# Kernel tuning notes

Hardware: AMD Instinct MI355X
Metric: run time of the kernel (lower is better)

Reference implementation:

```python
import jax, jax.numpy as jnp
import numpy as np

D_MODEL = 128
N_HEADS = 8
HEAD_DIM = D_MODEL // N_HEADS
N_NODES = 50000
N_EDGES = 640000


def setup_inputs() -> dict:
    key = jax.random.key(0)
    ks = jax.random.split(key, 10)
    sd = 1.0 / np.sqrt(D_MODEL)
    return {
        "node_embeds": jax.random.normal(ks[0], (N_NODES, D_MODEL), dtype=jnp.float32),
        "edge_index": jax.random.randint(ks[1], (2, N_EDGES), 0, N_NODES, dtype=jnp.int64),
        "Wq": jax.random.uniform(ks[2], (D_MODEL, D_MODEL), jnp.float32, -sd, sd),
        "bq": jax.random.uniform(ks[3], (D_MODEL,), jnp.float32, -sd, sd),
        "Wk": jax.random.uniform(ks[4], (D_MODEL, D_MODEL), jnp.float32, -sd, sd),
        "bk": jax.random.uniform(ks[5], (D_MODEL,), jnp.float32, -sd, sd),
        "Wv": jax.random.uniform(ks[6], (D_MODEL, D_MODEL), jnp.float32, -sd, sd),
        "bv": jax.random.uniform(ks[7], (D_MODEL,), jnp.float32, -sd, sd),
        "gamma": jnp.ones((D_MODEL,), jnp.float32),
        "beta": jnp.zeros((D_MODEL,), jnp.float32),
    }


def reference(node_embeds, edge_index, Wq, bq, Wk, bk, Wv, bv, gamma, beta):
    num_nodes = node_embeds.shape[0]
    rows, cols = edge_index[0], edge_index[1]
    src = node_embeds[rows]  # (E, d)
    tgt = node_embeds[cols]  # (E, d)
    q = (src @ Wq.T + bq).reshape(-1, N_HEADS, HEAD_DIM)
    k = (tgt @ Wk.T + bk).reshape(-1, N_HEADS, HEAD_DIM)
    v = (tgt @ Wv.T + bv).reshape(-1, N_HEADS, HEAD_DIM)
    att = jnp.einsum('ehd,ehd->eh', q, k) / jnp.sqrt(jnp.float32(HEAD_DIM))
    exp_att = jnp.exp(jnp.clip(att, -10.0, 10.0))  # (E, h)
    att_sum = jax.ops.segment_sum(exp_att, rows, num_segments=num_nodes)  # (N, h)
    att_norm = exp_att / (att_sum[rows] + 1e-8)
    weighted_v = (att_norm[..., None] * v).reshape(-1, D_MODEL)  # (E, d)
    out = jax.ops.segment_sum(weighted_v, rows, num_segments=num_nodes)
    out = out + node_embeds
    # LayerNorm, eps=1e-6
    mu = jnp.mean(out, axis=-1, keepdims=True)
    var = jnp.mean(jnp.square(out - mu), axis=-1, keepdims=True)
    out = (out - mu) * jax.lax.rsqrt(var + 1e-6) * gamma + beta
    return out
```

## Files before the change

kernel.cpp:

```cpp
#include <hip/hip_runtime.h>
#include <hip/hip_bf16.h>
#include <cstdint>

#define D_MODEL 128
#define N_HEADS 8
#define HEAD_DIM 16

typedef __attribute__((ext_vector_type(8))) short bf16x8;
typedef __attribute__((ext_vector_type(4))) float f32x4;

static __device__ __forceinline__ float b2f(unsigned short u) {
  unsigned int x = ((unsigned int)u) << 16;
  return __builtin_bit_cast(float, x);
}
static __device__ __forceinline__ unsigned short f2b(float f) {
  __hip_bfloat16 h = __float2bfloat16(f);
  return __builtin_bit_cast(unsigned short, h);
}

__global__ __launch_bounds__(256) void cvtw_kernel(
    const float* __restrict__ Wq, const float* __restrict__ Wk,
    const float* __restrict__ Wv, unsigned short* __restrict__ Wb)
{
  const int wb = blockIdx.x;
  const int m  = wb >> 3;
  const float* src = (m == 0) ? Wq : (m == 1) ? Wk : Wv;
  unsigned short* dst = Wb + (size_t)m * 16384;
  const int base = ((wb & 7) * 256 + threadIdx.x) * 8;
  const float4 a = reinterpret_cast<const float4*>(src + base)[0];
  const float4 c = reinterpret_cast<const float4*>(src + base)[1];
  unsigned short tmp[8];
  tmp[0] = f2b(a.x); tmp[1] = f2b(a.y); tmp[2] = f2b(a.z); tmp[3] = f2b(a.w);
  tmp[4] = f2b(c.x); tmp[5] = f2b(c.y); tmp[6] = f2b(c.z); tmp[7] = f2b(c.w);
  reinterpret_cast<uint4*>(dst + base)[0] = *reinterpret_cast<uint4*>(tmp);
}

__global__ __launch_bounds__(128) void qkv_mfma(
    const float* __restrict__ X, const unsigned short* __restrict__ Wb,
    const float* __restrict__ bq, const float* __restrict__ bk,
    const float* __restrict__ bv,
    unsigned short* __restrict__ Qo, unsigned short* __restrict__ Ko,
    unsigned short* __restrict__ Vo, int N)
{
  __shared__ unsigned short Wl[128 * 128];
  const int t    = threadIdx.x;
  const int wave = t >> 6;
  const int l    = t & 63;
  const int lr   = l & 15;
  const int lg   = l >> 4;
  const int nw   = blockIdx.x * 64 + wave * 32;

  bf16x8 a[2][4];
  #pragma unroll
  for (int ng = 0; ng < 2; ++ng) {
    const int arow = nw + ng * 16 + lr;
    if (arow < N) {
      const float* xp = X + (size_t)arow * D_MODEL + lg * 8;
      #pragma unroll
      for (int ks = 0; ks < 4; ++ks) {
        const float4 f0 = reinterpret_cast<const float4*>(xp + ks * 32)[0];
        const float4 f1 = reinterpret_cast<const float4*>(xp + ks * 32)[1];
        unsigned short tm[8];
        tm[0] = f2b(f0.x); tm[1] = f2b(f0.y); tm[2] = f2b(f0.z); tm[3] = f2b(f0.w);
        tm[4] = f2b(f1.x); tm[5] = f2b(f1.y); tm[6] = f2b(f1.z); tm[7] = f2b(f1.w);
        a[ng][ks] = *reinterpret_cast<bf16x8*>(tm);
      }
    } else {
      #pragma unroll
      for (int ks = 0; ks < 4; ++ks) a[ng][ks] = bf16x8{0,0,0,0,0,0,0,0};
    }
  }

  const float* biases[3] = {bq, bk, bv};
  unsigned short* outs[3] = {Qo, Ko, Vo};

  #pragma unroll 1
  for (int m = 0; m < 3; ++m) {
    __syncthreads();
    {
      const uint4* wsrc = reinterpret_cast<const uint4*>(Wb + (size_t)m * 16384);
      uint4* wl4 = reinterpret_cast<uint4*>(Wl);
      #pragma unroll
      for (int i = 0; i < 16; ++i) {
        const int cg = i * 128 + t;
        const int r  = cg >> 4;
        const int j  = cg & 15;
        wl4[r * 16 + (j ^ (r & 7))] = wsrc[cg];
      }
    }
    __syncthreads();

    unsigned short* __restrict__ O = outs[m];
    const float* __restrict__ bias = biases[m];
    float bias8[8];
    #pragma unroll
    for (int c = 0; c < 8; ++c) bias8[c] = bias[c * 16 + lr];

    #pragma unroll
    for (int c = 0; c < 8; ++c) {
      const int row = c * 16 + lr;
      bf16x8 w[4];
      #pragma unroll
      for (int ks = 0; ks < 4; ++ks) {
        const int j = ks * 4 + lg;
        w[ks] = *reinterpret_cast<const bf16x8*>(
            Wl + ((row * 16 + (j ^ (row & 7))) * 8));
      }
      #pragma unroll
      for (int ng = 0; ng < 2; ++ng) {
        f32x4 acc = {bias8[c], bias8[c], bias8[c], bias8[c]};
        #pragma unroll
        for (int ks = 0; ks < 4; ++ks)
          acc = __builtin_amdgcn_mfma_f32_16x16x32_bf16(a[ng][ks], w[ks], acc, 0, 0, 0);
        #pragma unroll
        for (int r = 0; r < 4; ++r) {
          const int orow = nw + ng * 16 + lg * 4 + r;
          if (orow < N) O[(size_t)orow * D_MODEL + c * 16 + lr] = f2b(acc[r]);
        }
      }
    }
  }
}

__global__ __launch_bounds__(256) void hist_kernel(
    const int* __restrict__ rows, int* __restrict__ cnt, int E)
{
  const int e = blockIdx.x * 256 + threadIdx.x;
  if (e < E) atomicAdd(&cnt[rows[e]], 1);
}

__global__ __launch_bounds__(256) void partial_kernel(
    const int* __restrict__ cnt, int* __restrict__ bsum, int N)
{
  __shared__ int wsum[4];
  const int t = threadIdx.x;
  const int base = blockIdx.x * 1024 + t * 4;
  int s = 0;
  #pragma unroll
  for (int i = 0; i < 4; ++i)
    if (base + i < N) s += cnt[base + i];
  #pragma unroll
  for (int off = 32; off > 0; off >>= 1) s += __shfl_xor(s, off, 64);
  if ((t & 63) == 0) wsum[t >> 6] = s;
  __syncthreads();
  if (t == 0) bsum[blockIdx.x] = wsum[0] + wsum[1] + wsum[2] + wsum[3];
}

__global__ __launch_bounds__(256) void scansums_kernel(
    const int* __restrict__ bsum, int* __restrict__ boff, int nb)
{
  __shared__ int p[256];
  __shared__ int carry_s;
  const int t = threadIdx.x;
  if (t == 0) carry_s = 0;
  __syncthreads();
  for (int c0 = 0; c0 < nb; c0 += 256) {
    const int v = (c0 + t < nb) ? bsum[c0 + t] : 0;
    p[t] = v;
    __syncthreads();
    for (int off = 1; off < 256; off <<= 1) {
      const int other = (t >= off) ? p[t - off] : 0;
      __syncthreads();
      p[t] += other;
      __syncthreads();
    }
    const int carry = carry_s;
    if (c0 + t < nb) boff[c0 + t] = carry + p[t] - v;
    __syncthreads();
    if (t == 0) carry_s = carry + p[255];
    __syncthreads();
  }
}

__global__ __launch_bounds__(256) void emit_kernel(
    const int* __restrict__ cnt, const int* __restrict__ boff,
    int* __restrict__ row_ptr, int* __restrict__ row_cur, int N, int E)
{
  __shared__ int psum[256];
  const int t = threadIdx.x;
  const int base = blockIdx.x * 1024 + t * 4;
  int v[4];
  #pragma unroll
  for (int i = 0; i < 4; ++i)
    v[i] = (base + i < N) ? cnt[base + i] : 0;
  const int local = v[0] + v[1] + v[2] + v[3];
  psum[t] = local;
  __syncthreads();
  for (int off = 1; off < 256; off <<= 1) {
    const int other = (t >= off) ? psum[t - off] : 0;
    __syncthreads();
    psum[t] += other;
    __syncthreads();
  }
  int pre = boff[blockIdx.x] + psum[t] - local;
  #pragma unroll
  for (int i = 0; i < 4; ++i) {
    const int idx = base + i;
    if (idx < N) {
      row_ptr[idx] = pre;
      row_cur[idx] = pre;
      pre += v[i];
    }
  }
  if (blockIdx.x == 0 && t == 0) row_ptr[N] = E;
}

__global__ __launch_bounds__(256) void scatter_kernel(
    const int* __restrict__ rows, const int* __restrict__ cols,
    int* __restrict__ row_cur, int* __restrict__ csr_cols, int E)
{
  const int e = blockIdx.x * 256 + threadIdx.x;
  if (e >= E) return;
  const int pos = atomicAdd(&row_cur[rows[e]], 1);
  csr_cols[pos] = cols[e];
}

__global__ __launch_bounds__(256) void fused_kernel(
    const unsigned short* __restrict__ Q, const unsigned short* __restrict__ K,
    const unsigned short* __restrict__ V, const float* __restrict__ X,
    const int* __restrict__ row_ptr, const int* __restrict__ csr_cols,
    const float* __restrict__ gamma, const float* __restrict__ beta,
    float* __restrict__ out, int N)
{
  __shared__ float lds[4][576];
  const int wv = threadIdx.x >> 6;
  const int n  = blockIdx.x * 4 + wv;
  if (n >= N) return;
  const int l  = threadIdx.x & 63;
  const int h  = l & 7;
  const int g  = l >> 3;
  const int hd = l >> 3;

  unsigned* __restrict__ Vu = reinterpret_cast<unsigned*>(lds[wv]);
  float*    __restrict__ El = lds[wv] + 512;

  float qf[16];
  {
    const unsigned short* qp = Q + (size_t)n * D_MODEL + h * HEAD_DIM;
    const bf16x8 q0 = *reinterpret_cast<const bf16x8*>(qp);
    const bf16x8 q1 = *reinterpret_cast<const bf16x8*>(qp + 8);
    #pragma unroll
    for (int i = 0; i < 8; ++i) {
      qf[i]     = b2f((unsigned short)q0[i]);
      qf[8 + i] = b2f((unsigned short)q1[i]);
    }
  }

  float accx = 0.f, accy = 0.f, dlane = 0.f;
  const int e0 = row_ptr[n];
  const int e1 = row_ptr[n + 1];

  const int rcol = (l & 7) * 64;
  const int rrot = (l >> 3) + 4 * (l & 7);

  for (int eb = e0; eb < e1; eb += 8) {
    const int  eg    = eb + g;
    const bool valid = eg < e1;
    const int  c     = valid ? csr_cols[eg] : 0;

    const unsigned short* kp = K + (size_t)c * D_MODEL + h * HEAD_DIM;
    const unsigned short* vp = V + (size_t)c * D_MODEL + h * HEAD_DIM;
    const bf16x8 k0 = *reinterpret_cast<const bf16x8*>(kp);
    const bf16x8 k1 = *reinterpret_cast<const bf16x8*>(kp + 8);
    const bf16x8 v0 = *reinterpret_cast<const bf16x8*>(vp);
    const bf16x8 v1 = *reinterpret_cast<const bf16x8*>(vp + 8);

    float s = 0.f;
    #pragma unroll
    for (int i = 0; i < 8; ++i) {
      s = fmaf(qf[i],     b2f((unsigned short)k0[i]), s);
      s = fmaf(qf[8 + i], b2f((unsigned short)k1[i]), s);
    }
    s *= 0.25f;
    s = fminf(fmaxf(s, -10.f), 10.f);
    const float ea = valid ? __expf(s) : 0.f;
    dlane += ea;

    El[l] = ea;
    {
      const uint4 u0 = __builtin_bit_cast(uint4, v0);
      const uint4 u1 = __builtin_bit_cast(uint4, v1);
      Vu[0 * 64 + ((l +  0) & 63)] = u0.x;
      Vu[1 * 64 + ((l +  4) & 63)] = u0.y;
      Vu[2 * 64 + ((l +  8) & 63)] = u0.z;
      Vu[3 * 64 + ((l + 12) & 63)] = u0.w;
      Vu[4 * 64 + ((l + 16) & 63)] = u1.x;
      Vu[5 * 64 + ((l + 20) & 63)] = u1.y;
      Vu[6 * 64 + ((l + 24) & 63)] = u1.z;
      Vu[7 * 64 + ((l + 28) & 63)] = u1.w;
    }
    __builtin_amdgcn_sched_barrier(0);

    #pragma unroll
    for (int j = 0; j < 8; ++j) {
      const float    aj = El[j * 8 + hd];
      const unsigned vv = Vu[rcol + ((j * 8 + rrot) & 63)];
      accx = fmaf(aj, b2f((unsigned short)(vv & 0xffffu)), accx);
      accy = fmaf(aj, b2f((unsigned short)(vv >> 16)), accy);
    }
    __builtin_amdgcn_sched_barrier(0);
  }

  dlane += __shfl_xor(dlane, 8,  64);
  dlane += __shfl_xor(dlane, 16, 64);
  dlane += __shfl_xor(dlane, 32, 64);
  const float denom = __shfl(dlane, hd, 64);

  const float inv = 1.f / (denom + 1e-8f);
  const float2 x = reinterpret_cast<const float2*>(X + (size_t)n * D_MODEL)[l];
  const float a0 = accx * inv + x.x;
  const float a1 = accy * inv + x.y;

  float sm = a0 + a1;
  float ss = a0 * a0 + a1 * a1;
  #pragma unroll
  for (int off = 32; off > 0; off >>= 1) {
    sm += __shfl_xor(sm, off, 64);
    ss += __shfl_xor(ss, off, 64);
  }
  const float mean = sm * (1.f / 128.f);
  const float var  = ss * (1.f / 128.f) - mean * mean;
  const float rs   = rsqrtf(var + 1e-6f);
  const float2 gm = reinterpret_cast<const float2*>(gamma)[l];
  const float2 bt = reinterpret_cast<const float2*>(beta)[l];
  float2 o;
  o.x = (a0 - mean) * rs * gm.x + bt.x;
  o.y = (a1 - mean) * rs * gm.y + bt.y;
  reinterpret_cast<float2*>(out + (size_t)n * D_MODEL)[l] = o;
}

extern "C" void kernel_launch(void* const* d_in, const int* in_sizes, int n_in,
                              void* d_out, int out_size, void* d_ws, size_t ws_size,
                              hipStream_t stream)
{
  const float* X     = (const float*)d_in[0];
  const int*   ei    = (const int*)  d_in[1];
  const float* Wq    = (const float*)d_in[2];
  const float* bq    = (const float*)d_in[3];
  const float* Wk    = (const float*)d_in[4];
  const float* bk    = (const float*)d_in[5];
  const float* Wv    = (const float*)d_in[6];
  const float* bv    = (const float*)d_in[7];
  const float* gamma = (const float*)d_in[8];
  const float* beta  = (const float*)d_in[9];

  const int N = in_sizes[0] / D_MODEL;
  const int E = in_sizes[1] / 2;
  const int* rows = ei;
  const int* cols = ei + E;

  const size_t nd = (size_t)N * D_MODEL;
  unsigned short* Wb = (unsigned short*)d_ws;
  unsigned short* Qb = Wb + 3 * 16384;
  unsigned short* Kb = Qb + nd;
  unsigned short* Vb = Kb + nd;
  int* row_cnt  = (int*)(Vb + nd);
  int* row_ptr  = row_cnt + N;
  int* row_cur  = row_ptr + N + 1;
  int* csr_cols = row_cur + N;
  int* bsum     = csr_cols + E;
  int* boff     = bsum + ((N + 1023) / 1024) + 1;

  const int nb = (N + 1023) / 1024;

  hipMemsetAsync(row_cnt, 0, (size_t)N * sizeof(int), stream);

  cvtw_kernel<<<24, 256, 0, stream>>>(Wq, Wk, Wv, Wb);

  hist_kernel<<<(E + 255) / 256, 256, 0, stream>>>(rows, row_cnt, E);
  partial_kernel<<<nb, 256, 0, stream>>>(row_cnt, bsum, N);
  scansums_kernel<<<1, 256, 0, stream>>>(bsum, boff, nb);
  emit_kernel<<<nb, 256, 0, stream>>>(row_cnt, boff, row_ptr, row_cur, N, E);
  scatter_kernel<<<(E + 255) / 256, 256, 0, stream>>>(rows, cols, row_cur, csr_cols, E);

  qkv_mfma<<<(N + 63) / 64, 128, 0, stream>>>(
      X, Wb, bq, bk, bv, Qb, Kb, Vb, N);

  fused_kernel<<<(N + 3) / 4, 256, 0, stream>>>(
      Qb, Kb, Vb, X, row_ptr, csr_cols, gamma, beta, (float*)d_out, N);
}
```

Before: 164.0 us.

## Software-pipeline edge gathers with prefetch of next K/V and column indices

Restructures the per-node edge loop so the K/V gathers for the next batch of 8 edges, and the column indices two batches ahead, are issued before the current batch's LDS exchange and accumulation. The LDS scratch is doubled and ping-ponged between iterations. The aim is to hide the global-memory gather latency behind compute within a single wave. It costs more registers for the in-flight K/V vectors, which may reduce occupancy, and loads past the last batch fall back to row 0.

```diff
diff --git a/kernel.cpp b/kernel.cpp
--- a/kernel.cpp
+++ b/kernel.cpp
@@ -222,7 +222,7 @@
     const float* __restrict__ gamma, const float* __restrict__ beta,
     float* __restrict__ out, int N)
 {
-  __shared__ float lds[4][576];
+  __shared__ float lds[4][2][576];
   const int wv = threadIdx.x >> 6;
   const int n  = blockIdx.x * 4 + wv;
   if (n >= N) return;
@@ -231,8 +231,8 @@
   const int g  = l >> 3;
   const int hd = l >> 3;
 
-  unsigned* __restrict__ Vu = reinterpret_cast<unsigned*>(lds[wv]);
-  float*    __restrict__ El = lds[wv] + 512;
+  float* buf0 = lds[wv][0];
+  float* buf1 = lds[wv][1];
 
   float qf[16];
   {
@@ -253,52 +253,82 @@
   const int rcol = (l & 7) * 64;
   const int rrot = (l >> 3) + 4 * (l & 7);
 
-  for (int eb = e0; eb < e1; eb += 8) {
-    const int  eg    = eb + g;
-    const bool valid = eg < e1;
-    const int  c     = valid ? csr_cols[eg] : 0;
-
-    const unsigned short* kp = K + (size_t)c * D_MODEL + h * HEAD_DIM;
-    const unsigned short* vp = V + (size_t)c * D_MODEL + h * HEAD_DIM;
-    const bf16x8 k0 = *reinterpret_cast<const bf16x8*>(kp);
-    const bf16x8 k1 = *reinterpret_cast<const bf16x8*>(kp + 8);
-    const bf16x8 v0 = *reinterpret_cast<const bf16x8*>(vp);
-    const bf16x8 v1 = *reinterpret_cast<const bf16x8*>(vp + 8);
-
-    float s = 0.f;
-    #pragma unroll
-    for (int i = 0; i < 8; ++i) {
-      s = fmaf(qf[i],     b2f((unsigned short)k0[i]), s);
-      s = fmaf(qf[8 + i], b2f((unsigned short)k1[i]), s);
-    }
-    s *= 0.25f;
-    s = fminf(fmaxf(s, -10.f), 10.f);
-    const float ea = valid ? __expf(s) : 0.f;
-    dlane += ea;
-
-    El[l] = ea;
+  if (e0 < e1) {
+    int cA;
+    bf16x8 kA0, kA1, vA0, vA1;
     {
-      const uint4 u0 = __builtin_bit_cast(uint4, v0);
-      const uint4 u1 = __builtin_bit_cast(uint4, v1);
-      Vu[0 * 64 + ((l +  0) & 63)] = u0.x;
-      Vu[1 * 64 + ((l +  4) & 63)] = u0.y;
-      Vu[2 * 64 + ((l +  8) & 63)] = u0.z;
-      Vu[3 * 64 + ((l + 12) & 63)] = u0.w;
-      Vu[4 * 64 + ((l + 16) & 63)] = u1.x;
-      Vu[5 * 64 + ((l + 20) & 63)] = u1.y;
-      Vu[6 * 64 + ((l + 24) & 63)] = u1.z;
-      Vu[7 * 64 + ((l + 28) & 63)] = u1.w;
-    }
-    __builtin_amdgcn_sched_barrier(0);
-
-    #pragma unroll
-    for (int j = 0; j < 8; ++j) {
-      const float    aj = El[j * 8 + hd];
-      const unsigned vv = Vu[rcol + ((j * 8 + rrot) & 63)];
-      accx = fmaf(aj, b2f((unsigned short)(vv & 0xffffu)), accx);
-      accy = fmaf(aj, b2f((unsigned short)(vv >> 16)), accy);
-    }
-    __builtin_amdgcn_sched_barrier(0);
+      const int eg = e0 + g;
+      cA = (eg < e1) ? csr_cols[eg] : 0;
+      const unsigned short* kp = K + (size_t)cA * D_MODEL + h * HEAD_DIM;
+      const unsigned short* vp = V + (size_t)cA * D_MODEL + h * HEAD_DIM;
+      kA0 = *reinterpret_cast<const bf16x8*>(kp);
+      kA1 = *reinterpret_cast<const bf16x8*>(kp + 8);
+      vA0 = *reinterpret_cast<const bf16x8*>(vp);
+      vA1 = *reinterpret_cast<const bf16x8*>(vp + 8);
+    }
+    int cB = 0;
+    if (e0 + 8 < e1) {
+      const int eg = e0 + 8 + g;
+      cB = (eg < e1) ? csr_cols[eg] : 0;
+    }
+
+    for (int eb = e0; eb < e1; eb += 8) {
+      const bool valid = (eb + g) < e1;
+      float s = 0.f;
+      #pragma unroll
+      for (int i = 0; i < 8; ++i) {
+        s = fmaf(qf[i],     b2f((unsigned short)kA0[i]), s);
+        s = fmaf(qf[8 + i], b2f((unsigned short)kA1[i]), s);
+      }
+      s *= 0.25f;
+      s = fminf(fmaxf(s, -10.f), 10.f);
+      const float ea = valid ? __expf(s) : 0.f;
+      dlane += ea;
+
+      bf16x8 kB0, kB1, vB0, vB1;
+      {
+        const unsigned short* kp = K + (size_t)cB * D_MODEL + h * HEAD_DIM;
+        const unsigned short* vp = V + (size_t)cB * D_MODEL + h * HEAD_DIM;
+        kB0 = *reinterpret_cast<const bf16x8*>(kp);
+        kB1 = *reinterpret_cast<const bf16x8*>(kp + 8);
+        vB0 = *reinterpret_cast<const bf16x8*>(vp);
+        vB1 = *reinterpret_cast<const bf16x8*>(vp + 8);
+      }
+      int cC = 0;
+      if (eb + 16 < e1) {
+        const int eg = eb + 16 + g;
+        cC = (eg < e1) ? csr_cols[eg] : 0;
+      }
+
+      float*    El = buf0 + 512;
+      unsigned* Vu = reinterpret_cast<unsigned*>(buf0);
+      El[l] = ea;
+      {
+        const uint4 u0 = __builtin_bit_cast(uint4, vA0);
+        const uint4 u1 = __builtin_bit_cast(uint4, vA1);
+        Vu[0 * 64 + ((l +  0) & 63)] = u0.x;
+        Vu[1 * 64 + ((l +  4) & 63)] = u0.y;
+        Vu[2 * 64 + ((l +  8) & 63)] = u0.z;
+        Vu[3 * 64 + ((l + 12) & 63)] = u0.w;
+        Vu[4 * 64 + ((l + 16) & 63)] = u1.x;
+        Vu[5 * 64 + ((l + 20) & 63)] = u1.y;
+        Vu[6 * 64 + ((l + 24) & 63)] = u1.z;
+        Vu[7 * 64 + ((l + 28) & 63)] = u1.w;
+      }
+      __builtin_amdgcn_sched_barrier(0);
+
+      #pragma unroll
+      for (int j = 0; j < 8; ++j) {
+        const float    aj = El[j * 8 + hd];
+        const unsigned vv = Vu[rcol + ((j * 8 + rrot) & 63)];
+        accx = fmaf(aj, b2f((unsigned short)(vv & 0xffffu)), accx);
+        accy = fmaf(aj, b2f((unsigned short)(vv >> 16)), accy);
+      }
+
+      cB = cC;
+      kA0 = kB0; kA1 = kB1; vA0 = vB0; vA1 = vB1;
+      float* tmp = buf0; buf0 = buf1; buf1 = tmp;
+    }
   }
 
   dlane += __shfl_xor(dlane, 8,  64);
```

Measured after the change: 167.3 us. 2.0% more time.

## Accumulate V per lane in registers and reduce with shuffles instead of LDS

Applied to the files above, without the earlier changes.

Lanes now map head-major (h = l>>3, edge group = l&7), and each lane accumulates its full 16-wide head slice of weighted V in registers. A shuffle reduction across the 8 edge lanes runs at the end, replacing the per-iteration LDS transpose of V and exp weights. The next edge's column index is also prefetched one iteration ahead. This removes LDS traffic and the per-edge-block shared-memory round trips, at the cost of more registers (16 accumulators) and an end-of-node reduction of 16 values over 3 shuffle stages.

```diff
diff --git a/kernel.cpp b/kernel.cpp
--- a/kernel.cpp
+++ b/kernel.cpp
@@ -222,17 +222,11 @@
     const float* __restrict__ gamma, const float* __restrict__ beta,
     float* __restrict__ out, int N)
 {
-  __shared__ float lds[4][576];
-  const int wv = threadIdx.x >> 6;
-  const int n  = blockIdx.x * 4 + wv;
+  const int n = blockIdx.x * 4 + (threadIdx.x >> 6);
   if (n >= N) return;
-  const int l  = threadIdx.x & 63;
-  const int h  = l & 7;
-  const int g  = l >> 3;
-  const int hd = l >> 3;
-
-  unsigned* __restrict__ Vu = reinterpret_cast<unsigned*>(lds[wv]);
-  float*    __restrict__ El = lds[wv] + 512;
+  const int l = threadIdx.x & 63;
+  const int h = l >> 3;
+  const int g = l & 7;
 
   float qf[16];
   {
@@ -246,17 +240,27 @@
     }
   }
 
-  float accx = 0.f, accy = 0.f, dlane = 0.f;
+  float acc[16];
+  #pragma unroll
+  for (int i = 0; i < 16; ++i) acc[i] = 0.f;
+  float dlane = 0.f;
+
   const int e0 = row_ptr[n];
   const int e1 = row_ptr[n + 1];
 
-  const int rcol = (l & 7) * 64;
-  const int rrot = (l >> 3) + 4 * (l & 7);
+  int cA = 0;
+  if (e0 < e1) {
+    const int eg = e0 + g;
+    cA = (eg < e1) ? csr_cols[eg] : 0;
+  }
 
   for (int eb = e0; eb < e1; eb += 8) {
-    const int  eg    = eb + g;
-    const bool valid = eg < e1;
-    const int  c     = valid ? csr_cols[eg] : 0;
+    const bool valid = (eb + g) < e1;
+    const int  c     = cA;
+    {
+      const int eg2 = eb + 8 + g;
+      cA = (eg2 < e1) ? csr_cols[eg2] : 0;
+    }
 
     const unsigned short* kp = K + (size_t)c * D_MODEL + h * HEAD_DIM;
     const unsigned short* vp = V + (size_t)c * D_MODEL + h * HEAD_DIM;
@@ -276,40 +280,30 @@
     const float ea = valid ? __expf(s) : 0.f;
     dlane += ea;
 
-    El[l] = ea;
-    {
-      const uint4 u0 = __builtin_bit_cast(uint4, v0);
-      const uint4 u1 = __builtin_bit_cast(uint4, v1);
-      Vu[0 * 64 + ((l +  0) & 63)] = u0.x;
-      Vu[1 * 64 + ((l +  4) & 63)] = u0.y;
-      Vu[2 * 64 + ((l +  8) & 63)] = u0.z;
-      Vu[3 * 64 + ((l + 12) & 63)] = u0.w;
-      Vu[4 * 64 + ((l + 16) & 63)] = u1.x;
-      Vu[5 * 64 + ((l + 20) & 63)] = u1.y;
-      Vu[6 * 64 + ((l + 24) & 63)] = u1.z;
-      Vu[7 * 64 + ((l + 28) & 63)] = u1.w;
-    }
-    __builtin_amdgcn_sched_barrier(0);
-
-    #pragma unroll
-    for (int j = 0; j < 8; ++j) {
-      const float    aj = El[j * 8 + hd];
-      const unsigned vv = Vu[rcol + ((j * 8 + rrot) & 63)];
-      accx = fmaf(aj, b2f((unsigned short)(vv & 0xffffu)), accx);
-      accy = fmaf(aj, b2f((unsigned short)(vv >> 16)), accy);
-    }
-    __builtin_amdgcn_sched_barrier(0);
-  }
-
-  dlane += __shfl_xor(dlane, 8,  64);
-  dlane += __shfl_xor(dlane, 16, 64);
-  dlane += __shfl_xor(dlane, 32, 64);
-  const float denom = __shfl(dlane, hd, 64);
-
-  const float inv = 1.f / (denom + 1e-8f);
+    #pragma unroll
+    for (int i = 0; i < 8; ++i) {
+      acc[i]     = fmaf(ea, b2f((unsigned short)v0[i]), acc[i]);
+      acc[8 + i] = fmaf(ea, b2f((unsigned short)v1[i]), acc[8 + i]);
+    }
+  }
+
+  #pragma unroll
+  for (int off = 1; off <= 4; off <<= 1) {
+    dlane += __shfl_xor(dlane, off, 64);
+    #pragma unroll
+    for (int i = 0; i < 16; ++i) acc[i] += __shfl_xor(acc[i], off, 64);
+  }
+
+  float num0 = acc[0], num1 = acc[1];
+  #pragma unroll
+  for (int j = 1; j < 8; ++j) {
+    if (g == j) { num0 = acc[2 * j]; num1 = acc[2 * j + 1]; }
+  }
+
+  const float inv = 1.f / (dlane + 1e-8f);
   const float2 x = reinterpret_cast<const float2*>(X + (size_t)n * D_MODEL)[l];
-  const float a0 = accx * inv + x.x;
-  const float a1 = accy * inv + x.y;
+  const float a0 = num0 * inv + x.x;
+  const float a1 = num1 * inv + x.y;
 
   float sm = a0 + a1;
   float ss = a0 * a0 + a1 * a1;
```

Result: slower. 172.1 us (+5.0%).
